# Performance work log

Hardware: AMD Instinct MI355X
Metric: run time of the kernel (lower is better)

Reference implementation:

```python
import jax, jax.numpy as jnp
import numpy as np
import math

B, TQ, TK, D, I, H = 2, 2048, 2048, 2048, 2048, 16
HD = I // H  # head dim = 128
PAD = 128    # trailing keys treated as padding


def setup_inputs() -> dict:
    key = jax.random.key(0)
    ks = jax.random.split(key, 12)
    s_in = 1.0 / math.sqrt(D)
    s_i = 1.0 / math.sqrt(I)
    inp = {
        "query_states": jax.random.normal(ks[0], (B, TQ, D), jnp.float32),
        "kv_states": jax.random.normal(ks[1], (B, TK, D), jnp.float32),
        # pad the trailing PAD key positions (True = masked out)
        "kv_padding_mask": jnp.broadcast_to(jnp.arange(TK) >= (TK - PAD), (B, TK)),
        "Wq": jax.random.normal(ks[2], (I, D), jnp.float32) * s_in,
        "bq": jnp.zeros((I,), jnp.float32),
        "Wk": jax.random.normal(ks[3], (I, D), jnp.float32) * s_in,
        "bk": jnp.zeros((I,), jnp.float32),
        "Wv": jax.random.normal(ks[4], (I, D), jnp.float32) * s_in,
        "bv": jnp.zeros((I,), jnp.float32),
        "Wo": jax.random.normal(ks[5], (D, I), jnp.float32) * s_i,
        "bo": jnp.zeros((D,), jnp.float32),
        "gate": jnp.zeros((D,), jnp.float32),
    }
    return inp


def _split_heads(x):
    b, t, _ = x.shape
    return x.reshape(b, t, H, HD).transpose(0, 2, 1, 3)  # (B,H,T,HD)


def reference(query_states, kv_states, kv_padding_mask, Wq, bq, Wk, bk, Wv, bv, Wo, bo, gate):
    q = _split_heads(query_states @ Wq.T + bq)  # (B,H,Tq,HD)
    k = _split_heads(kv_states @ Wk.T + bk)     # (B,H,Tk,HD)
    v = _split_heads(kv_states @ Wv.T + bv)     # (B,H,Tk,HD)

    scores = jnp.einsum("bhqd,bhkd->bhqk", q, k) / jnp.sqrt(jnp.float32(HD))
    causal = jnp.triu(jnp.ones((TQ, TK), bool), k=1)  # True above diagonal
    neg_inf = jnp.float32(-jnp.inf)
    scores = jnp.where(causal[None, None, :, :], neg_inf, scores)
    scores = jnp.where(kv_padding_mask[:, None, None, :], neg_inf, scores)

    probs = jax.nn.softmax(scores, axis=-1)  # dropout p=0 -> identity
    ctx = jnp.einsum("bhqk,bhkd->bhqd", probs, v)
    ctx = ctx.transpose(0, 2, 1, 3).reshape(B, TQ, I)  # merge heads
    ctx = ctx @ Wo.T + bo
    ctx = ctx * jax.nn.sigmoid(gate)  # gated residual, gate init 0 -> 0.5
    return query_states + ctx
```

## Files before the change

kernel.cpp:

```cpp
#include <hip/hip_runtime.h>
#include <hip/hip_bf16.h>
#include <stdint.h>

#define B_N   2
#define T_Q   2048
#define T_K   2048
#define D_IN  2048
#define I_IN  2048
#define H_N   16
#define HD_N  128

using bf16 = __hip_bfloat16;
typedef short bf16x8 __attribute__((ext_vector_type(8)));
typedef float floatx4 __attribute__((ext_vector_type(4)));

__device__ __forceinline__ void async_copy16(const void* gsrc, void* ldst) {
    __builtin_amdgcn_global_load_lds(
        (const __attribute__((address_space(1))) void*)gsrc,
        (__attribute__((address_space(3))) void*)ldst, 16, 0, 0);
}

__device__ __forceinline__ floatx4 mfma_bf16(bf16x8 a, bf16x8 b, floatx4 c) {
    return __builtin_amdgcn_mfma_f32_16x16x32_bf16(a, b, c, 0, 0, 0);
}

#define XG 1048576
#define WG 524288
struct CastArgs {
    const float *s0, *s1, *s2, *s3, *s4, *s5;
    bf16 *d0, *d1, *d2, *d3, *d4, *d5;
};
__global__ void cast_all(CastArgs a) {
    int g = blockIdx.x * 256 + threadIdx.x;
    const float* src; bf16* dst; size_t off;
    if (g < XG)            { src = a.s0; dst = a.d0; off = (size_t)g * 8; }
    else if (g < 2 * XG)   { src = a.s1; dst = a.d1; off = (size_t)(g - XG) * 8; }
    else {
        int r = g - 2 * XG, s = r >> 19;
        off = (size_t)(r & (WG - 1)) * 8;
        src = (s == 0) ? a.s2 : (s == 1) ? a.s3 : (s == 2) ? a.s4 : a.s5;
        dst = (s == 0) ? a.d2 : (s == 1) ? a.d3 : (s == 2) ? a.d4 : a.d5;
    }
    float4 x = *((const float4*)(src + off));
    float4 y = *((const float4*)(src + off + 4));
    union { bf16x8 v; bf16 h[8]; } u;
    u.h[0] = __float2bfloat16(x.x); u.h[1] = __float2bfloat16(x.y);
    u.h[2] = __float2bfloat16(x.z); u.h[3] = __float2bfloat16(x.w);
    u.h[4] = __float2bfloat16(y.x); u.h[5] = __float2bfloat16(y.y);
    u.h[6] = __float2bfloat16(y.z); u.h[7] = __float2bfloat16(y.w);
    *((bf16x8*)(dst + off)) = u.v;
}


#define GEMM_SETUP(APTR, WPTR, KDIM)                                            \
    __shared__ bf16 sAls[3][256 * 64];                                          \
    __shared__ bf16 sBls[3][128 * 64];                                          \
    bf16 *aC = &sAls[0][0], *aN = &sAls[1][0], *aP = &sAls[2][0];               \
    bf16 *bC = &sBls[0][0], *bN = &sBls[1][0], *bP = &sBls[2][0];               \
    const int tid  = threadIdx.x;                                               \
    const int wave = tid >> 6, lane = tid & 63;                                 \
    const int quad = lane >> 4, r16 = lane & 15;                                \
    const int wm = wave >> 1, wn = wave & 1;                                    \
    const int K  = (KDIM);                                                      \
    const int NT = (KDIM) / 64;                                                 \
    floatx4 acc[4][4];                                                          \
    _Pragma("unroll") for (int i = 0; i < 4; i++)                               \
      _Pragma("unroll") for (int j = 0; j < 4; j++)                             \
        acc[i][j] = (floatx4)(0.0f);                                            \
    const int p0 = tid, p1 = tid + 512, p2 = tid + 1024, p3 = tid + 1536;       \
    const bf16* srcA0 = (APTR) + (size_t)(m0 + (p0 >> 3)) * K + (((p0 & 7) ^ ((p0 >> 3) & 7)) * 8); \
    const bf16* srcA1 = (APTR) + (size_t)(m0 + (p1 >> 3)) * K + (((p1 & 7) ^ ((p1 >> 3) & 7)) * 8); \
    const bf16* srcA2 = (APTR) + (size_t)(m0 + (p2 >> 3)) * K + (((p2 & 7) ^ ((p2 >> 3) & 7)) * 8); \
    const bf16* srcA3 = (APTR) + (size_t)(m0 + (p3 >> 3)) * K + (((p3 & 7) ^ ((p3 >> 3) & 7)) * 8); \
    const bf16* srcB0 = (WPTR) + (size_t)(n0 + (p0 >> 3)) * K + (((p0 & 7) ^ ((p0 >> 3) & 7)) * 8); \
    const bf16* srcB1 = (WPTR) + (size_t)(n0 + (p1 >> 3)) * K + (((p1 & 7) ^ ((p1 >> 3) & 7)) * 8); \
    const int dA0 = p0 * 8, dA1 = p1 * 8, dA2 = p2 * 8, dA3 = p3 * 8;           \
    const int dB0 = p0 * 8, dB1 = p1 * 8;                                       \
    int offA[4][2], offB[4][2];                                                 \
    _Pragma("unroll") for (int mt = 0; mt < 4; mt++)                            \
      _Pragma("unroll") for (int ks = 0; ks < 2; ks++)                          \
        offA[mt][ks] = (wm*64 + mt*16 + r16) * 64 + (((ks*4 + quad) ^ (r16 & 7)) * 8); \
    _Pragma("unroll") for (int nt = 0; nt < 4; nt++)                            \
      _Pragma("unroll") for (int ks = 0; ks < 2; ks++)                          \
        offB[nt][ks] = (wn*64 + nt*16 + r16) * 64 + (((ks*4 + quad) ^ (r16 & 7)) * 8)

#define GEMM_PROLOGUE()                                                         \
    async_copy16(srcA0,      aC + dA0);                                         \
    async_copy16(srcA1,      aC + dA1);                                         \
    async_copy16(srcA2,      aC + dA2);                                         \
    async_copy16(srcA3,      aC + dA3);                                         \
    async_copy16(srcB0,      bC + dB0);                                         \
    async_copy16(srcB1,      bC + dB1);                                         \
    async_copy16(srcA0 + 64, aN + dA0);                                         \
    async_copy16(srcA1 + 64, aN + dA1);                                         \
    async_copy16(srcA2 + 64, aN + dA2);                                         \
    async_copy16(srcA3 + 64, aN + dA3);                                         \
    async_copy16(srcB0 + 64, bN + dB0);                                         \
    async_copy16(srcB1 + 64, bN + dB1);                                         \
    asm volatile("s_waitcnt vmcnt(6)" ::: "memory");                            \
    asm volatile("s_barrier" ::: "memory")

#define GEMM_TILE_BODY()                                                        \
  do {                                                                          \
    const int kp = (t + 2) * 64;                                                \
    const bool pre = (t < NT - 2);                                              \
    bf16x8 aF[2][2], bF[4][2], aG[2][2];                                        \
    _Pragma("unroll") for (int ks = 0; ks < 2; ks++) {                          \
      aF[0][ks] = *(const bf16x8*)(aC + offA[0][ks]);                           \
      aF[1][ks] = *(const bf16x8*)(aC + offA[1][ks]);                           \
      bF[0][ks] = *(const bf16x8*)(bC + offB[0][ks]);                           \
      bF[1][ks] = *(const bf16x8*)(bC + offB[1][ks]);                           \
      bF[2][ks] = *(const bf16x8*)(bC + offB[2][ks]);                           \
      bF[3][ks] = *(const bf16x8*)(bC + offB[3][ks]);                           \
    }                                                                           \
    if (pre) {                                                                  \
      async_copy16(srcA0 + kp, aP + dA0);                                       \
      async_copy16(srcA1 + kp, aP + dA1);                                       \
      async_copy16(srcA2 + kp, aP + dA2);                                       \
    }                                                                           \
    asm volatile("s_barrier" ::: "memory");                                     \
    asm volatile("s_waitcnt lgkmcnt(0)" ::: "memory");                          \
    __builtin_amdgcn_sched_barrier(0);                                          \
    __builtin_amdgcn_s_setprio(1);                                              \
    _Pragma("unroll") for (int ks = 0; ks < 2; ks++)                            \
      _Pragma("unroll") for (int mi = 0; mi < 2; mi++)                          \
        _Pragma("unroll") for (int ni = 0; ni < 4; ni++)                        \
          acc[mi][ni] = mfma_bf16(aF[mi][ks], bF[ni][ks], acc[mi][ni]);         \
    __builtin_amdgcn_s_setprio(0);                                              \
    asm volatile("s_barrier" ::: "memory");                                     \
    _Pragma("unroll") for (int ks = 0; ks < 2; ks++) {                          \
      aG[0][ks] = *(const bf16x8*)(aC + offA[2][ks]);                           \
      aG[1][ks] = *(const bf16x8*)(aC + offA[3][ks]);                           \
    }                                                                           \
    if (pre) {                                                                  \
      async_copy16(srcA3 + kp, aP + dA3);                                       \
      async_copy16(srcB0 + kp, bP + dB0);                                       \
      async_copy16(srcB1 + kp, bP + dB1);                                       \
    }                                                                           \
    if (pre)                 asm volatile("s_waitcnt vmcnt(6)" ::: "memory");   \
    else if (t == NT - 2)    asm volatile("s_waitcnt vmcnt(0)" ::: "memory");   \
    asm volatile("s_barrier" ::: "memory");                                     \
    asm volatile("s_waitcnt lgkmcnt(0)" ::: "memory");                          \
    __builtin_amdgcn_sched_barrier(0);                                          \
    __builtin_amdgcn_s_setprio(1);                                              \
    _Pragma("unroll") for (int ks = 0; ks < 2; ks++)                            \
      _Pragma("unroll") for (int mi = 0; mi < 2; mi++)                          \
        _Pragma("unroll") for (int ni = 0; ni < 4; ni++)                        \
          acc[2+mi][ni] = mfma_bf16(aG[mi][ks], bF[ni][ks], acc[2+mi][ni]);     \
    __builtin_amdgcn_s_setprio(0);                                              \
    asm volatile("s_barrier" ::: "memory");                                     \
    bf16* tmpA = aC; aC = aN; aN = aP; aP = tmpA;                               \
    bf16* tmpB = bC; bC = bN; bN = bP; bP = tmpB;                               \
  } while (0)

__global__ __launch_bounds__(512, 2) void qkv_gemm(
    const bf16* __restrict__ xq, const bf16* __restrict__ xkv,
    const bf16* __restrict__ wq, const bf16* __restrict__ wk, const bf16* __restrict__ wv,
    const float* __restrict__ bq, const float* __restrict__ bk, const float* __restrict__ bv,
    bf16* __restrict__ qo, bf16* __restrict__ ko, bf16* __restrict__ vt)
{
    const int m0  = blockIdx.x * 256;
    const int seg = blockIdx.y >> 4;
    const int n0  = (blockIdx.y & 15) * 128;
    const bf16*  Ag   = (seg == 0) ? xq : xkv;
    const bf16*  Wg   = (seg == 0) ? wq : (seg == 1) ? wk : wv;
    const float* bias = (seg == 0) ? bq : (seg == 1) ? bk : bv;

    GEMM_SETUP(Ag, Wg, D_IN);
    GEMM_PROLOGUE();
    for (int t = 0; t < NT; t++) GEMM_TILE_BODY();

    if (seg < 2) {
        bf16* Cb = (seg == 0) ? qo : ko;
        #pragma unroll
        for (int mt = 0; mt < 4; mt++)
            #pragma unroll
            for (int nt = 0; nt < 4; nt++) {
                int col = n0 + wn*64 + nt*16 + r16;
                float bs = bias[col];
                #pragma unroll
                for (int r = 0; r < 4; r++) {
                    size_t row = (size_t)(m0 + wm*64 + mt*16 + quad*4 + r);
                    Cb[row*I_IN + col] = __float2bfloat16(acc[mt][nt][r] + bs);
                }
            }
    } else {
        #pragma unroll
        for (int mt = 0; mt < 4; mt++)
            #pragma unroll
            for (int nt = 0; nt < 4; nt++) {
                int col = n0 + wn*64 + nt*16 + r16;
                float bs = bias[col];
                int hh = col >> 7, dd = col & 127;
                int m  = m0 + wm*64 + mt*16 + quad*4;
                int bb = m >> 11, tt = m & 2047;
                union { ushort4 u; bf16 h[4]; } pk;
                #pragma unroll
                for (int r = 0; r < 4; r++) pk.h[r] = __float2bfloat16(acc[mt][nt][r] + bs);
                *((ushort4*)(vt + ((size_t)((bb*16 + hh)*128 + dd))*T_K + tt)) = pk.u;
            }
    }
}

__global__ __launch_bounds__(256, 2) void flash_attn(
    const bf16* __restrict__ Q,
    const bf16* __restrict__ Km,
    const bf16* __restrict__ Vt,
    bf16* __restrict__ Ctx)
{
    __shared__ bf16 sK[2][64 * 128];
    __shared__ bf16 sV[2][128 * 64];
    __shared__ bf16 sP[64 * 80];

    const int tid  = threadIdx.x;
    const int wave = tid >> 6, lane = tid & 63;
    const int quad = lane >> 4, r16 = lane & 15;
    const int n  = blockIdx.x;
    const int bh = n & 31, qt = 31 - (n >> 5);
    const int b  = bh >> 4, h = bh & 15;

    const bf16* Qbase = Q + ((size_t)(b*T_Q) + qt*64 + wave*16) * I_IN + h*HD_N;
    bf16x8 qf[4];
    #pragma unroll
    for (int ks = 0; ks < 4; ks++)
        qf[ks] = *(const bf16x8*)(Qbase + (size_t)r16*I_IN + ks*32 + quad*8);

    floatx4 acc_o[8];
    #pragma unroll
    for (int nt = 0; nt < 8; nt++) acc_o[nt] = (floatx4)(0.0f);
    float m2[4], l[4];
    #pragma unroll
    for (int r = 0; r < 4; r++) { m2[r] = -3.0e38f; l[r] = 0.0f; }

    const int kend = (qt < 29) ? qt : 29;
    const bf16* Kb0 = Km + (size_t)(b*T_K) * I_IN + h*HD_N;
    const bf16* Vb0 = Vt + (size_t)bh * HD_N * T_K;
    const float c1 = 0.08838834764831845f * 1.4426950408889634f;

    {
        #pragma unroll
        for (int i = 0; i < 4; i++) {
            int c = wave*256 + i*64 + lane;
            int row = c >> 4, cc = (c & 15) ^ (row & 15);
            async_copy16(Kb0 + (size_t)row*I_IN + cc*8, &sK[0][c*8]);
        }
        #pragma unroll
        for (int i = 0; i < 4; i++) {
            int c = wave*256 + i*64 + lane;
            int row = c >> 3, cc = (c & 7) ^ (row & 7);
            async_copy16(Vb0 + (size_t)row*T_K + cc*8, &sV[0][c*8]);
        }
    }

    for (int kt = 0; kt <= kend; kt++) {
        const int cur = kt & 1;
        if (kt < kend) {
            const int nxt = cur ^ 1;
            #pragma unroll
            for (int i = 0; i < 4; i++) {
                int c = wave*256 + i*64 + lane;
                int row = c >> 4, cc = (c & 15) ^ (row & 15);
                async_copy16(Kb0 + (size_t)((kt+1)*64 + row)*I_IN + cc*8, &sK[nxt][c*8]);
            }
            #pragma unroll
            for (int i = 0; i < 4; i++) {
                int c = wave*256 + i*64 + lane;
                int row = c >> 3, cc = (c & 7) ^ (row & 7);
                async_copy16(Vb0 + (size_t)row*T_K + (kt+1)*64 + cc*8, &sV[nxt][c*8]);
            }
            asm volatile("s_waitcnt vmcnt(8)\n\ts_barrier" ::: "memory");
        } else {
            asm volatile("s_waitcnt vmcnt(0)\n\ts_barrier" ::: "memory");
        }

        floatx4 sacc[4];
        #pragma unroll
        for (int nt = 0; nt < 4; nt++) sacc[nt] = (floatx4)(0.0f);
        #pragma unroll
        for (int ks = 0; ks < 4; ks++) {
            bf16x8 bk[4];
            #pragma unroll
            for (int nt = 0; nt < 4; nt++) {
                int key = nt*16 + r16;
                int cc  = (ks*4 + quad) ^ r16;
                bk[nt] = *(const bf16x8*)(&sK[cur][key*128 + cc*8]);
            }
            #pragma unroll
            for (int nt = 0; nt < 4; nt++)
                sacc[nt] = mfma_bf16(qf[ks], bk[nt], sacc[nt]);
        }

        const bool diag = (kt == qt);
        float tv[4][4];
        #pragma unroll
        for (int nt = 0; nt < 4; nt++)
            #pragma unroll
            for (int r = 0; r < 4; r++) {
                float v = sacc[nt][r] * c1;
                if (diag && (nt*16 + r16 > wave*16 + quad*4 + r)) v = -1.0e30f;
                tv[nt][r] = v;
            }

        #pragma unroll
        for (int r = 0; r < 4; r++) {
            float mx = tv[0][r];
            #pragma unroll
            for (int nt = 1; nt < 4; nt++) mx = fmaxf(mx, tv[nt][r]);
            mx = fmaxf(mx, __shfl_xor(mx, 1, 64));
            mx = fmaxf(mx, __shfl_xor(mx, 2, 64));
            mx = fmaxf(mx, __shfl_xor(mx, 4, 64));
            mx = fmaxf(mx, __shfl_xor(mx, 8, 64));
            float mn = fmaxf(m2[r], mx);
            float alpha = exp2f(m2[r] - mn);
            m2[r] = mn;
            float rs = 0.0f;
            int prow = wave*16 + quad*4 + r;
            #pragma unroll
            for (int nt = 0; nt < 4; nt++) {
                float p = exp2f(tv[nt][r] - mn);
                rs += p;
                sP[prow*80 + nt*16 + r16] = __float2bfloat16(p);
            }
            rs += __shfl_xor(rs, 1, 64);
            rs += __shfl_xor(rs, 2, 64);
            rs += __shfl_xor(rs, 4, 64);
            rs += __shfl_xor(rs, 8, 64);
            l[r] = l[r]*alpha + rs;
            #pragma unroll
            for (int nt = 0; nt < 8; nt++) acc_o[nt][r] *= alpha;
        }

        #pragma unroll
        for (int ks2 = 0; ks2 < 2; ks2++) {
            bf16x8 ap = *(const bf16x8*)(&sP[(wave*16 + r16)*80 + ks2*32 + quad*8]);
            #pragma unroll
            for (int nt = 0; nt < 8; nt++) {
                int d  = nt*16 + r16;
                int cc = (ks2*4 + quad) ^ (d & 7);
                bf16x8 bv = *(const bf16x8*)(&sV[cur][d*64 + cc*8]);
                acc_o[nt] = mfma_bf16(ap, bv, acc_o[nt]);
            }
        }

        asm volatile("s_waitcnt lgkmcnt(0)\n\ts_barrier" ::: "memory");
    }

    bf16* Cb = Ctx + ((size_t)(b*T_Q) + qt*64 + wave*16) * I_IN + h*HD_N;
    #pragma unroll
    for (int r = 0; r < 4; r++) {
        float inv = 1.0f / l[r];
        #pragma unroll
        for (int nt = 0; nt < 8; nt++)
            Cb[(size_t)(quad*4 + r)*I_IN + nt*16 + r16] =
                __float2bfloat16(acc_o[nt][r] * inv);
    }
}

__global__ __launch_bounds__(512, 2) void gemm_final(
    const bf16* __restrict__ A, const bf16* __restrict__ W,
    const float* __restrict__ bias, const float* __restrict__ gate,
    const float* __restrict__ resid, float* __restrict__ Cf)
{
    const int m0 = blockIdx.x * 256;
    const int n0 = blockIdx.y * 128;

    GEMM_SETUP(A, W, I_IN);
    GEMM_PROLOGUE();
    for (int t = 0; t < NT; t++) GEMM_TILE_BODY();

    const int N = D_IN;
    #pragma unroll
    for (int mt = 0; mt < 4; mt++)
        #pragma unroll
        for (int nt = 0; nt < 4; nt++) {
            int col = n0 + wn*64 + nt*16 + r16;
            float bs = bias[col];
            float g  = gate[col];
            float sg = 1.0f / (1.0f + exp2f(-g * 1.4426950408889634f));
            #pragma unroll
            for (int r = 0; r < 4; r++) {
                size_t row = (size_t)(m0 + wm*64 + mt*16 + quad*4 + r);
                Cf[row*N + col] = resid[row*N + col] + sg * (acc[mt][nt][r] + bs);
            }
        }
}

extern "C" void kernel_launch(void* const* d_in, const int* in_sizes, int n_in,
                              void* d_out, int out_size, void* d_ws, size_t ws_size,
                              hipStream_t stream)
{
    const float* qs   = (const float*)d_in[0];
    const float* kvs  = (const float*)d_in[1];
    const float* Wq   = (const float*)d_in[3];
    const float* bq   = (const float*)d_in[4];
    const float* Wk   = (const float*)d_in[5];
    const float* bk   = (const float*)d_in[6];
    const float* Wv   = (const float*)d_in[7];
    const float* bv   = (const float*)d_in[8];
    const float* Wo   = (const float*)d_in[9];
    const float* bo   = (const float*)d_in[10];
    const float* gate = (const float*)d_in[11];
    float* out = (float*)d_out;

    bf16* ws = (bf16*)d_ws;
    const size_t WSZ = (size_t)I_IN * D_IN;
    const size_t XSZ = (size_t)B_N * T_Q * D_IN;
    bf16* wq_b  = ws;
    bf16* wk_b  = wq_b + WSZ;
    bf16* wv_b  = wk_b + WSZ;
    bf16* wo_b  = wv_b + WSZ;
    bf16* xq_b  = wo_b + WSZ;
    bf16* xkv_b = xq_b + XSZ;
    bf16* q_b   = xkv_b + XSZ;
    bf16* k_b   = q_b + XSZ;
    bf16* vt_b  = k_b + XSZ;
    bf16* ctx_b = xq_b;

    CastArgs ca;
    ca.s0 = qs;  ca.d0 = xq_b;
    ca.s1 = kvs; ca.d1 = xkv_b;
    ca.s2 = Wq;  ca.d2 = wq_b;
    ca.s3 = Wk;  ca.d3 = wk_b;
    ca.s4 = Wv;  ca.d4 = wv_b;
    ca.s5 = Wo;  ca.d5 = wo_b;
    cast_all<<<16384, 256, 0, stream>>>(ca);

    qkv_gemm<<<dim3(16, 48), 512, 0, stream>>>(xq_b, xkv_b, wq_b, wk_b, wv_b,
                                               bq, bk, bv, q_b, k_b, vt_b);

    flash_attn<<<1024, 256, 0, stream>>>(q_b, k_b, vt_b, ctx_b);

    gemm_final<<<dim3(16, 16), 512, 0, stream>>>(ctx_b, wo_b, bo, gate, qs, out);
}
```

Before: 419.7 us.

## Rewrite QKV GEMM with 256-thread blocks and lazy softmax rescaling in attention

The QKV projection GEMM becomes a standalone kernel with 256 threads, each wave owning a 128x64 output tile (32 accumulators), and a K-step of 32 with a triple-buffered async LDS pipeline. This gives more MFMA work per LDS fragment load, at the cost of higher register pressure and fewer waves per block. Separately, flash attention now rescales the running max and output accumulator only when some row's new max exceeds the stored max by more than 8 (log2 units). This skips the per-tile alpha exp and the 32 accumulator multiplies in most iterations, but lets probabilities reach up to 2^8 before rescaling, which may affect bf16 precision.

```diff
diff --git a/kernel.cpp b/kernel.cpp
--- a/kernel.cpp
+++ b/kernel.cpp
@@ -51,6 +51,127 @@
     *((bf16x8*)(dst + off)) = u.v;
 }
 
+
+__global__ __launch_bounds__(256, 2) void qkv_gemm(
+    const bf16* __restrict__ xq, const bf16* __restrict__ xkv,
+    const bf16* __restrict__ wq, const bf16* __restrict__ wk, const bf16* __restrict__ wv,
+    const float* __restrict__ bq, const float* __restrict__ bk, const float* __restrict__ bv,
+    bf16* __restrict__ qo, bf16* __restrict__ ko, bf16* __restrict__ vt)
+{
+    __shared__ bf16 sA[3][256 * 32];
+    __shared__ bf16 sB[3][128 * 32];
+    bf16 *aC = &sA[0][0], *aN = &sA[1][0], *aP = &sA[2][0];
+    bf16 *bC = &sB[0][0], *bN = &sB[1][0], *bP = &sB[2][0];
+    const int tid  = threadIdx.x;
+    const int wave = tid >> 6, lane = tid & 63;
+    const int quad = lane >> 4, r16 = lane & 15;
+    const int wm = wave >> 1, wn = wave & 1;
+    const int m0  = blockIdx.x * 256;
+    const int seg = blockIdx.y >> 4;
+    const int n0  = (blockIdx.y & 15) * 128;
+    const int K   = D_IN;
+    const int NT  = K / 32;
+
+    const bf16*  Ag   = (seg == 0) ? xq : xkv;
+    const bf16*  Wg   = (seg == 0) ? wq : (seg == 1) ? wk : wv;
+    const float* bias = (seg == 0) ? bq : (seg == 1) ? bk : bv;
+
+    floatx4 acc[8][4];
+    #pragma unroll
+    for (int i = 0; i < 8; i++)
+        #pragma unroll
+        for (int j = 0; j < 4; j++) acc[i][j] = (floatx4)(0.0f);
+
+    const int pa0 = tid, pa1 = tid + 256, pa2 = tid + 512, pa3 = tid + 768;
+    const bf16* srcA0 = Ag + (size_t)(m0 + (pa0 >> 2)) * K + (((pa0 & 3) ^ ((pa0 >> 4) & 3)) * 8);
+    const bf16* srcA1 = Ag + (size_t)(m0 + (pa1 >> 2)) * K + (((pa1 & 3) ^ ((pa1 >> 4) & 3)) * 8);
+    const bf16* srcA2 = Ag + (size_t)(m0 + (pa2 >> 2)) * K + (((pa2 & 3) ^ ((pa2 >> 4) & 3)) * 8);
+    const bf16* srcA3 = Ag + (size_t)(m0 + (pa3 >> 2)) * K + (((pa3 & 3) ^ ((pa3 >> 4) & 3)) * 8);
+    const bf16* srcB0 = Wg + (size_t)(n0 + (pa0 >> 2)) * K + (((pa0 & 3) ^ ((pa0 >> 4) & 3)) * 8);
+    const bf16* srcB1 = Wg + (size_t)(n0 + (pa1 >> 2)) * K + (((pa1 & 3) ^ ((pa1 >> 4) & 3)) * 8);
+    const int dA0 = pa0 * 8, dA1 = pa1 * 8, dA2 = pa2 * 8, dA3 = pa3 * 8;
+    const int dB0 = pa0 * 8, dB1 = pa1 * 8;
+
+    const int sw = (r16 >> 2) & 3;
+    int offA[8], offB[4];
+    #pragma unroll
+    for (int mt = 0; mt < 8; mt++)
+        offA[mt] = (wm*128 + mt*16 + r16) * 32 + ((quad ^ sw) * 8);
+    #pragma unroll
+    for (int nt = 0; nt < 4; nt++)
+        offB[nt] = (wn*64 + nt*16 + r16) * 32 + ((quad ^ sw) * 8);
+
+    async_copy16(srcA0,      aC + dA0);
+    async_copy16(srcA1,      aC + dA1);
+    async_copy16(srcA2,      aC + dA2);
+    async_copy16(srcA3,      aC + dA3);
+    async_copy16(srcB0,      bC + dB0);
+    async_copy16(srcB1,      bC + dB1);
+    async_copy16(srcA0 + 32, aN + dA0);
+    async_copy16(srcA1 + 32, aN + dA1);
+    async_copy16(srcA2 + 32, aN + dA2);
+    async_copy16(srcA3 + 32, aN + dA3);
+    async_copy16(srcB0 + 32, bN + dB0);
+    async_copy16(srcB1 + 32, bN + dB1);
+
+    for (int t = 0; t < NT; t++) {
+        if (t < NT - 1) asm volatile("s_waitcnt vmcnt(6)" ::: "memory");
+        else            asm volatile("s_waitcnt vmcnt(0)" ::: "memory");
+        asm volatile("s_barrier" ::: "memory");
+        if (t < NT - 2) {
+            const int kp = (t + 2) * 32;
+            async_copy16(srcA0 + kp, aP + dA0);
+            async_copy16(srcA1 + kp, aP + dA1);
+            async_copy16(srcA2 + kp, aP + dA2);
+            async_copy16(srcA3 + kp, aP + dA3);
+            async_copy16(srcB0 + kp, bP + dB0);
+            async_copy16(srcB1 + kp, bP + dB1);
+        }
+        bf16x8 aF[8], bF[4];
+        #pragma unroll
+        for (int mt = 0; mt < 8; mt++) aF[mt] = *(const bf16x8*)(aC + offA[mt]);
+        #pragma unroll
+        for (int nt = 0; nt < 4; nt++) bF[nt] = *(const bf16x8*)(bC + offB[nt]);
+        #pragma unroll
+        for (int mt = 0; mt < 8; mt++)
+            #pragma unroll
+            for (int nt = 0; nt < 4; nt++)
+                acc[mt][nt] = mfma_bf16(aF[mt], bF[nt], acc[mt][nt]);
+        bf16* tmpA = aC; aC = aN; aN = aP; aP = tmpA;
+        bf16* tmpB = bC; bC = bN; bN = bP; bP = tmpB;
+    }
+
+    if (seg < 2) {
+        bf16* Cb = (seg == 0) ? qo : ko;
+        #pragma unroll
+        for (int mt = 0; mt < 8; mt++)
+            #pragma unroll
+            for (int nt = 0; nt < 4; nt++) {
+                int col = n0 + wn*64 + nt*16 + r16;
+                float bs = bias[col];
+                #pragma unroll
+                for (int r = 0; r < 4; r++) {
+                    size_t row = (size_t)(m0 + wm*128 + mt*16 + quad*4 + r);
+                    Cb[row*I_IN + col] = __float2bfloat16(acc[mt][nt][r] + bs);
+                }
+            }
+    } else {
+        #pragma unroll
+        for (int mt = 0; mt < 8; mt++)
+            #pragma unroll
+            for (int nt = 0; nt < 4; nt++) {
+                int col = n0 + wn*64 + nt*16 + r16;
+                float bs = bias[col];
+                int hh = col >> 7, dd = col & 127;
+                int m  = m0 + wm*128 + mt*16 + quad*4;
+                int bb = m >> 11, tt = m & 2047;
+                union { ushort4 u; bf16 h[4]; } pk;
+                #pragma unroll
+                for (int r = 0; r < 4; r++) pk.h[r] = __float2bfloat16(acc[mt][nt][r] + bs);
+                *((ushort4*)(vt + ((size_t)((bb*16 + hh)*128 + dd))*T_K + tt)) = pk.u;
+            }
+    }
+}
 
 #define GEMM_SETUP(APTR, WPTR, KDIM)                                            \
     __shared__ bf16 sAls[3][256 * 64];                                          \
@@ -153,55 +274,6 @@
     bf16* tmpB = bC; bC = bN; bN = bP; bP = tmpB;                               \
   } while (0)
 
-__global__ __launch_bounds__(512, 2) void qkv_gemm(
-    const bf16* __restrict__ xq, const bf16* __restrict__ xkv,
-    const bf16* __restrict__ wq, const bf16* __restrict__ wk, const bf16* __restrict__ wv,
-    const float* __restrict__ bq, const float* __restrict__ bk, const float* __restrict__ bv,
-    bf16* __restrict__ qo, bf16* __restrict__ ko, bf16* __restrict__ vt)
-{
-    const int m0  = blockIdx.x * 256;
-    const int seg = blockIdx.y >> 4;
-    const int n0  = (blockIdx.y & 15) * 128;
-    const bf16*  Ag   = (seg == 0) ? xq : xkv;
-    const bf16*  Wg   = (seg == 0) ? wq : (seg == 1) ? wk : wv;
-    const float* bias = (seg == 0) ? bq : (seg == 1) ? bk : bv;
-
-    GEMM_SETUP(Ag, Wg, D_IN);
-    GEMM_PROLOGUE();
-    for (int t = 0; t < NT; t++) GEMM_TILE_BODY();
-
-    if (seg < 2) {
-        bf16* Cb = (seg == 0) ? qo : ko;
-        #pragma unroll
-        for (int mt = 0; mt < 4; mt++)
-            #pragma unroll
-            for (int nt = 0; nt < 4; nt++) {
-                int col = n0 + wn*64 + nt*16 + r16;
-                float bs = bias[col];
-                #pragma unroll
-                for (int r = 0; r < 4; r++) {
-                    size_t row = (size_t)(m0 + wm*64 + mt*16 + quad*4 + r);
-                    Cb[row*I_IN + col] = __float2bfloat16(acc[mt][nt][r] + bs);
-                }
-            }
-    } else {
-        #pragma unroll
-        for (int mt = 0; mt < 4; mt++)
-            #pragma unroll
-            for (int nt = 0; nt < 4; nt++) {
-                int col = n0 + wn*64 + nt*16 + r16;
-                float bs = bias[col];
-                int hh = col >> 7, dd = col & 127;
-                int m  = m0 + wm*64 + mt*16 + quad*4;
-                int bb = m >> 11, tt = m & 2047;
-                union { ushort4 u; bf16 h[4]; } pk;
-                #pragma unroll
-                for (int r = 0; r < 4; r++) pk.h[r] = __float2bfloat16(acc[mt][nt][r] + bs);
-                *((ushort4*)(vt + ((size_t)((bb*16 + hh)*128 + dd))*T_K + tt)) = pk.u;
-            }
-    }
-}
-
 __global__ __launch_bounds__(256, 2) void flash_attn(
     const bf16* __restrict__ Q,
     const bf16* __restrict__ Km,
@@ -301,33 +373,60 @@
                 tv[nt][r] = v;
             }
 
+        float mx[4];
         #pragma unroll
         for (int r = 0; r < 4; r++) {
-            float mx = tv[0][r];
-            #pragma unroll
-            for (int nt = 1; nt < 4; nt++) mx = fmaxf(mx, tv[nt][r]);
-            mx = fmaxf(mx, __shfl_xor(mx, 1, 64));
-            mx = fmaxf(mx, __shfl_xor(mx, 2, 64));
-            mx = fmaxf(mx, __shfl_xor(mx, 4, 64));
-            mx = fmaxf(mx, __shfl_xor(mx, 8, 64));
-            float mn = fmaxf(m2[r], mx);
-            float alpha = exp2f(m2[r] - mn);
-            m2[r] = mn;
-            float rs = 0.0f;
-            int prow = wave*16 + quad*4 + r;
-            #pragma unroll
-            for (int nt = 0; nt < 4; nt++) {
-                float p = exp2f(tv[nt][r] - mn);
-                rs += p;
-                sP[prow*80 + nt*16 + r16] = __float2bfloat16(p);
-            }
-            rs += __shfl_xor(rs, 1, 64);
-            rs += __shfl_xor(rs, 2, 64);
-            rs += __shfl_xor(rs, 4, 64);
-            rs += __shfl_xor(rs, 8, 64);
-            l[r] = l[r]*alpha + rs;
-            #pragma unroll
-            for (int nt = 0; nt < 8; nt++) acc_o[nt][r] *= alpha;
+            float m_ = tv[0][r];
+            #pragma unroll
+            for (int nt = 1; nt < 4; nt++) m_ = fmaxf(m_, tv[nt][r]);
+            m_ = fmaxf(m_, __shfl_xor(m_, 1, 64));
+            m_ = fmaxf(m_, __shfl_xor(m_, 2, 64));
+            m_ = fmaxf(m_, __shfl_xor(m_, 4, 64));
+            m_ = fmaxf(m_, __shfl_xor(m_, 8, 64));
+            mx[r] = m_;
+        }
+
+        bool grow = (mx[0] > m2[0] + 8.0f) || (mx[1] > m2[1] + 8.0f) ||
+                    (mx[2] > m2[2] + 8.0f) || (mx[3] > m2[3] + 8.0f);
+        if (__any(grow)) {
+            #pragma unroll
+            for (int r = 0; r < 4; r++) {
+                float mn = fmaxf(m2[r], mx[r]);
+                float alpha = exp2f(m2[r] - mn);
+                m2[r] = mn;
+                float rs = 0.0f;
+                int prow = wave*16 + quad*4 + r;
+                #pragma unroll
+                for (int nt = 0; nt < 4; nt++) {
+                    float p = exp2f(tv[nt][r] - mn);
+                    rs += p;
+                    sP[prow*80 + nt*16 + r16] = __float2bfloat16(p);
+                }
+                rs += __shfl_xor(rs, 1, 64);
+                rs += __shfl_xor(rs, 2, 64);
+                rs += __shfl_xor(rs, 4, 64);
+                rs += __shfl_xor(rs, 8, 64);
+                l[r] = l[r]*alpha + rs;
+                #pragma unroll
+                for (int nt = 0; nt < 8; nt++) acc_o[nt][r] *= alpha;
+            }
+        } else {
+            #pragma unroll
+            for (int r = 0; r < 4; r++) {
+                float rs = 0.0f;
+                int prow = wave*16 + quad*4 + r;
+                #pragma unroll
+                for (int nt = 0; nt < 4; nt++) {
+                    float p = exp2f(tv[nt][r] - m2[r]);
+                    rs += p;
+                    sP[prow*80 + nt*16 + r16] = __float2bfloat16(p);
+                }
+                rs += __shfl_xor(rs, 1, 64);
+                rs += __shfl_xor(rs, 2, 64);
+                rs += __shfl_xor(rs, 4, 64);
+                rs += __shfl_xor(rs, 8, 64);
+                l[r] += rs;
+            }
         }
 
         #pragma unroll
@@ -425,7 +524,7 @@
     ca.s5 = Wo;  ca.d5 = wo_b;
     cast_all<<<16384, 256, 0, stream>>>(ca);
 
-    qkv_gemm<<<dim3(16, 48), 512, 0, stream>>>(xq_b, xkv_b, wq_b, wk_b, wv_b,
+    qkv_gemm<<<dim3(16, 48), 256, 0, stream>>>(xq_b, xkv_b, wq_b, wk_b, wv_b,
                                                bq, bk, bv, q_b, k_b, vt_b);
 
     flash_attn<<<1024, 256, 0, stream>>>(q_b, k_b, vt_b, ctx_b);
```

New measurement: 441.9 us. 1.05x slower.
